# Performance work log

Hardware: AMD Instinct MI355X
Metric: run time of the kernel (lower is better)

## Reference

```python
import jax, jax.numpy as jnp
import numpy as np

EPS = 1e-5

def _layer_norm(x, g, b):
    mu = jnp.mean(x, axis=-1, keepdims=True)
    var = jnp.mean((x - mu) ** 2, axis=-1, keepdims=True)
    return (x - mu) * jax.lax.rsqrt(var + EPS) * g + b


def setup_inputs() -> dict:
    key = jax.random.key(0)
    ks = jax.random.split(key, 16)
    D, F = 768, 3072
    s = 0.02
    def lin(k, din, dout):
        return jax.random.normal(k, (din, dout), jnp.float32) * s
    return {
        "x": jax.random.normal(ks[0], (2, 2048, D), jnp.float32),
        "wq": lin(ks[1], D, D), "bq": jnp.zeros((D,), jnp.float32),
        "wk": lin(ks[2], D, D), "bk": jnp.zeros((D,), jnp.float32),
        "wv": lin(ks[3], D, D), "bv": jnp.zeros((D,), jnp.float32),
        "wo": lin(ks[4], D, D), "bo": jnp.zeros((D,), jnp.float32),
        "w1": lin(ks[5], D, F), "b1": jnp.zeros((F,), jnp.float32),
        "w2": lin(ks[6], F, D), "b2": jnp.zeros((D,), jnp.float32),
        "g1": jnp.ones((D,), jnp.float32), "be1": jnp.zeros((D,), jnp.float32),
        "g2": jnp.ones((D,), jnp.float32), "be2": jnp.zeros((D,), jnp.float32),
    }


def reference(x, wq, bq, wk, bk, wv, bv, wo, bo, w1, b1, w2, b2, g1, be1, g2, be2):
    B, S, D = x.shape
    H = 12
    hd = D // H
    h = _layer_norm(x, g1, be1)
    # project and split heads: [B,S,D] -> [B,H,S,hd]
    def heads(y):
        return y.reshape(B, S, H, hd).transpose(0, 2, 1, 3)
    q = heads(h @ wq + bq)
    k = heads(h @ wk + bk)
    v = heads(h @ wv + bv)
    energy = jnp.einsum("bhqd,bhkd->bhqk", q, k) / np.sqrt(hd).astype(np.float32)
    attention = jax.nn.softmax(energy, axis=-1)
    # NOTE: source bug preserved — uses raw energy (not attention) for AV matmul
    ctx = jnp.einsum("bhqk,bhkd->bhqd", energy, v)
    ctx = ctx.transpose(0, 2, 1, 3).reshape(B, S, D)
    attn_out = ctx @ wo + bo
    x = x + attn_out
    h2 = _layer_norm(x, g2, be2)
    mlp = jax.nn.gelu(h2 @ w1 + b1, approximate=False) @ w2 + b2
    x = x + mlp
    return (x, attention)
```

## Files before the change

### kernel.cpp

```cpp
#include <hip/hip_runtime.h>
#include <cmath>

typedef __bf16 bf16;
typedef __bf16 bf16x8 __attribute__((ext_vector_type(8)));
typedef __bf16 bf16x4v __attribute__((ext_vector_type(4)));
typedef float f32x4 __attribute__((ext_vector_type(4)));

#define DEV __device__ __forceinline__

DEV void gld16(const void* g, void* l) {
  __builtin_amdgcn_global_load_lds((__attribute__((address_space(1))) void*)(g),
                                   (__attribute__((address_space(3))) void*)(l), 16, 0, 0);
}

DEV f32x4 mfma16(bf16x8 a, bf16x8 b, f32x4 c) {
  return __builtin_amdgcn_mfma_f32_16x16x32_bf16(a, b, c, 0, 0, 0);
}

__global__ __launch_bounds__(256) void ln_kernel(const float* __restrict__ x,
    const float* __restrict__ g, const float* __restrict__ be, bf16* __restrict__ h)
{
  const int row = blockIdx.x, t = threadIdx.x;
  const float* xr = x + (size_t)row * 768;
  float v0 = xr[t], v1 = xr[t + 256], v2 = xr[t + 512];
  float s = v0 + v1 + v2;
  float ss = v0 * v0 + v1 * v1 + v2 * v2;
#pragma unroll
  for (int m = 32; m >= 1; m >>= 1) { s += __shfl_xor(s, m); ss += __shfl_xor(ss, m); }
  __shared__ float ps[8];
  const int w = t >> 6;
  if ((t & 63) == 0) { ps[w] = s; ps[4 + w] = ss; }
  __syncthreads();
  s = ps[0] + ps[1] + ps[2] + ps[3];
  ss = ps[4] + ps[5] + ps[6] + ps[7];
  const float mu = s * (1.0f / 768.0f);
  const float var = ss * (1.0f / 768.0f) - mu * mu;
  const float rs = rsqrtf(var + 1e-5f);
  bf16* hr = h + (size_t)row * 768;
  hr[t]       = (bf16)((v0 - mu) * rs * g[t]       + be[t]);
  hr[t + 256] = (bf16)((v1 - mu) * rs * g[t + 256] + be[t + 256]);
  hr[t + 512] = (bf16)((v2 - mu) * rs * g[t + 512] + be[t + 512]);
}

__global__ __launch_bounds__(256) void transpose_w(const float* __restrict__ w,
    bf16* __restrict__ wT, int din, int dout)
{
  __shared__ __align__(16) float tw[64 * 68];
  const int t = threadIdx.x;
  const int n0 = blockIdx.x * 64, k0 = blockIdx.y * 64;
#pragma unroll
  for (int it = 0; it < 4; ++it) {
    const int slot = it * 256 + t;
    const int r = slot >> 4, c = slot & 15;
    *(f32x4*)(tw + r * 68 + c * 4) = *(const f32x4*)(w + (size_t)(k0 + r) * dout + n0 + c * 4);
  }
  __syncthreads();
#pragma unroll
  for (int it = 0; it < 2; ++it) {
    const int slot = it * 256 + t;
    const int n = slot >> 3, c = slot & 7;
    bf16x8 o;
#pragma unroll
    for (int j = 0; j < 8; ++j) o[j] = (bf16)tw[(c * 8 + j) * 68 + n];
    *(bf16x8*)(wT + (size_t)(n0 + n) * din + k0 + c * 8) = o;
  }
}

__global__ __launch_bounds__(256) void transpose_v(const bf16* __restrict__ v, bf16* __restrict__ vT)
{
  __shared__ __align__(16) bf16 tv[64 * 80];
  const int t = threadIdx.x;
  const int s0 = blockIdx.x * 64, bh = blockIdx.y;
  const bf16* vg = v + ((size_t)bh * 2048 + s0) * 64;
#pragma unroll
  for (int it = 0; it < 2; ++it) {
    const int slot = it * 256 + t;
    const int r = slot >> 3, c = slot & 7;
    *(bf16x8*)(tv + r * 80 + c * 8) = *(const bf16x8*)(vg + slot * 8);
  }
  __syncthreads();
  bf16* og = vT + (size_t)bh * 64 * 2048 + s0;
#pragma unroll
  for (int it = 0; it < 2; ++it) {
    const int slot = it * 256 + t;
    const int d = slot >> 3, c = slot & 7;
    bf16x8 o;
#pragma unroll
    for (int j = 0; j < 8; ++j) o[j] = tv[(c * 8 + j) * 80 + d];
    *(bf16x8*)(og + (size_t)d * 2048 + c * 8) = o;
  }
}

template <int MODE>
__global__ __launch_bounds__(256, 2) void gemm_bt(
    const bf16* __restrict__ A, const bf16* __restrict__ B, const int K,
    const float* __restrict__ bias0, const float* __restrict__ bias1,
    const float* __restrict__ bias2, const float* __restrict__ resid,
    float* __restrict__ outf, bf16* __restrict__ outb,
    bf16* __restrict__ kout, bf16* __restrict__ vout)
{
  __shared__ __align__(16) bf16 As[128 * 32];
  __shared__ __align__(16) bf16 Bs[128 * 32];
  const int t = threadIdx.x;
  const int m0 = blockIdx.y * 128, n0 = blockIdx.x * 128;
  const int w = t >> 6, lane = t & 63, l15 = lane & 15, quad = lane >> 4;
  const int wr = (w >> 1) * 64, wc = (w & 1) * 64;

  const f32x4 zero = {0.f, 0.f, 0.f, 0.f};
  f32x4 acc[4][4];
#pragma unroll
  for (int i = 0; i < 4; ++i)
#pragma unroll
    for (int j = 0; j < 4; ++j) acc[i][j] = zero;

  for (int k0 = 0; k0 < K; k0 += 32) {
#pragma unroll
    for (int j = 0; j < 2; ++j) {
      const int slot = j * 256 + t;
      const int row = slot >> 2, kc = slot & 3;
      gld16(A + (size_t)(m0 + row) * K + k0 + kc * 8, As + (size_t)(j * 256 + (t & 192)) * 8);
      gld16(B + (size_t)(n0 + row) * K + k0 + kc * 8, Bs + (size_t)(j * 256 + (t & 192)) * 8);
    }
    __syncthreads();
    bf16x8 af[4], bfr[4];
#pragma unroll
    for (int i = 0; i < 4; ++i) af[i] = *(const bf16x8*)(As + (wr + i * 16 + l15) * 32 + quad * 8);
#pragma unroll
    for (int i = 0; i < 4; ++i) bfr[i] = *(const bf16x8*)(Bs + (wc + i * 16 + l15) * 32 + quad * 8);
#pragma unroll
    for (int mi = 0; mi < 4; ++mi)
#pragma unroll
      for (int ni = 0; ni < 4; ++ni) acc[mi][ni] = mfma16(af[mi], bfr[ni], acc[mi][ni]);
    __syncthreads();
  }

  if constexpr (MODE == 0) {
    const int part = n0 / 768;
    const int cb = n0 - part * 768;
    const float* bp = part == 0 ? bias0 : (part == 1 ? bias1 : bias2);
    bf16* dst = part == 0 ? outb : (part == 1 ? kout : vout);
    float bias[4];
#pragma unroll
    for (int ni = 0; ni < 4; ++ni) bias[ni] = bp[cb + wc + ni * 16 + l15];
#pragma unroll
    for (int mi = 0; mi < 4; ++mi) {
      const int tok = m0 + wr + mi * 16 + quad * 4;
      const int b = tok >> 11, sIdx = tok & 2047;
#pragma unroll
      for (int ni = 0; ni < 4; ++ni) {
        const int c = cb + wc + ni * 16 + l15;
        const int head = c >> 6, d = c & 63;
        bf16* o = dst + (((size_t)b * 12 + head) * 2048 + sIdx) * 64 + d;
#pragma unroll
        for (int r = 0; r < 4; ++r) o[(size_t)r * 64] = (bf16)(acc[mi][ni][r] + bias[ni]);
      }
    }
  } else if constexpr (MODE == 1 || MODE == 3) {
    float bias[4];
#pragma unroll
    for (int ni = 0; ni < 4; ++ni) bias[ni] = bias0[n0 + wc + ni * 16 + l15];
#pragma unroll
    for (int mi = 0; mi < 4; ++mi) {
      const int row = m0 + wr + mi * 16 + quad * 4;
#pragma unroll
      for (int ni = 0; ni < 4; ++ni) {
        const int c = n0 + wc + ni * 16 + l15;
#pragma unroll
        for (int r = 0; r < 4; ++r) {
          const size_t idx = (size_t)(row + r) * 768 + c;
          outf[idx] = resid[idx] + acc[mi][ni][r] + bias[ni];
        }
      }
    }
  } else {
    float bias[4];
#pragma unroll
    for (int ni = 0; ni < 4; ++ni) bias[ni] = bias0[n0 + wc + ni * 16 + l15];
#pragma unroll
    for (int mi = 0; mi < 4; ++mi) {
      const int row = m0 + wr + mi * 16 + quad * 4;
#pragma unroll
      for (int ni = 0; ni < 4; ++ni) {
        const int c = n0 + wc + ni * 16 + l15;
#pragma unroll
        for (int r = 0; r < 4; ++r) {
          const size_t idx = (size_t)(row + r) * 3072 + c;
          const float gv = acc[mi][ni][r] + bias[ni];
          outb[idx] = (bf16)(0.5f * gv * (1.0f + erff(gv * 0.70710678118f)));
        }
      }
    }
  }
}

__global__ __launch_bounds__(256, 2) void attn_kernel(
    const bf16* __restrict__ q, const bf16* __restrict__ k,
    const bf16* __restrict__ vT, bf16* __restrict__ ctx,
    float* __restrict__ energy)
{
  __shared__ __align__(16) bf16 qs[128 * 64];
  __shared__ __align__(16) bf16 ks[64 * 64];
  __shared__ __align__(16) bf16 vs[64 * 64];
  __shared__ __align__(16) bf16 es[128 * 64];
  const int t = threadIdx.x, w = t >> 6, lane = t & 63;
  const int l15 = lane & 15, quad = lane >> 4;
  const int q0 = blockIdx.x * 128, bh = blockIdx.y;
  const int b = bh / 12, head = bh % 12;

  const bf16* qg = q + ((size_t)bh * 2048 + q0) * 64;
#pragma unroll
  for (int j = 0; j < 4; ++j) gld16(qg + (j * 256 + t) * 8, qs + (size_t)(j * 256 + (t & 192)) * 8);

  const f32x4 zero = {0.f, 0.f, 0.f, 0.f};
  f32x4 accc[2][4];
#pragma unroll
  for (int mi = 0; mi < 2; ++mi)
#pragma unroll
    for (int ni = 0; ni < 4; ++ni) accc[mi][ni] = zero;

  for (int kt = 0; kt < 32; ++kt) {
    const bf16* kg = k + ((size_t)bh * 2048 + kt * 64) * 64;
#pragma unroll
    for (int j = 0; j < 2; ++j) gld16(kg + (j * 256 + t) * 8, ks + (size_t)(j * 256 + (t & 192)) * 8);
    const bf16* vg = vT + (size_t)bh * 64 * 2048 + kt * 64;
#pragma unroll
    for (int j = 0; j < 2; ++j) {
      const int slot = j * 256 + t;
      const int d = slot >> 3, c = slot & 7;
      gld16(vg + (size_t)d * 2048 + c * 8, vs + (size_t)(j * 256 + (t & 192)) * 8);
    }
    __syncthreads();

    f32x4 e[2][4];
#pragma unroll
    for (int mi = 0; mi < 2; ++mi)
#pragma unroll
      for (int nj = 0; nj < 4; ++nj) e[mi][nj] = zero;
#pragma unroll
    for (int kk = 0; kk < 2; ++kk) {
      bf16x8 aq[2];
#pragma unroll
      for (int mi = 0; mi < 2; ++mi)
        aq[mi] = *(const bf16x8*)(qs + (w * 32 + mi * 16 + l15) * 64 + kk * 32 + quad * 8);
#pragma unroll
      for (int nj = 0; nj < 4; ++nj) {
        bf16x8 kb8 = *(const bf16x8*)(ks + (nj * 16 + l15) * 64 + kk * 32 + quad * 8);
#pragma unroll
        for (int mi = 0; mi < 2; ++mi) e[mi][nj] = mfma16(aq[mi], kb8, e[mi][nj]);
      }
    }
#pragma unroll
    for (int mi = 0; mi < 2; ++mi)
#pragma unroll
      for (int nj = 0; nj < 4; ++nj)
#pragma unroll
        for (int r = 0; r < 4; ++r)
          es[(w * 32 + mi * 16 + quad * 4 + r) * 64 + nj * 16 + l15] = (bf16)(e[mi][nj][r] * 0.125f);

    float* eg = energy + ((size_t)(bh * 2048 + q0 + w * 32)) * 2048 + kt * 64;
#pragma unroll
    for (int it = 0; it < 8; ++it) {
      const int slot = it * 64 + lane;
      const int r = slot >> 4, c4 = slot & 15;
      bf16x4v ev = *(const bf16x4v*)(es + (w * 32 + r) * 64 + c4 * 4);
      f32x4 o = {(float)ev[0], (float)ev[1], (float)ev[2], (float)ev[3]};
      *(f32x4*)(eg + (size_t)r * 2048 + c4 * 4) = o;
    }

#pragma unroll
    for (int kk = 0; kk < 2; ++kk) {
      bf16x8 ae[2];
#pragma unroll
      for (int mi = 0; mi < 2; ++mi)
        ae[mi] = *(const bf16x8*)(es + (w * 32 + mi * 16 + l15) * 64 + kk * 32 + quad * 8);
#pragma unroll
      for (int ni = 0; ni < 4; ++ni) {
        bf16x8 vb8 = *(const bf16x8*)(vs + (ni * 16 + l15) * 64 + kk * 32 + quad * 8);
#pragma unroll
        for (int mi = 0; mi < 2; ++mi) accc[mi][ni] = mfma16(ae[mi], vb8, accc[mi][ni]);
      }
    }
    __syncthreads();
  }

#pragma unroll
  for (int mi = 0; mi < 2; ++mi) {
    const int srow = q0 + w * 32 + mi * 16 + quad * 4;
#pragma unroll
    for (int ni = 0; ni < 4; ++ni) {
      const int d = ni * 16 + l15;
      bf16* o = ctx + ((size_t)(b * 2048 + srow)) * 768 + head * 64 + d;
#pragma unroll
      for (int r = 0; r < 4; ++r) o[(size_t)r * 768] = (bf16)accc[mi][ni][r];
    }
  }
}

__global__ __launch_bounds__(256) void softmax_kernel(float* __restrict__ att)
{
  const int w = threadIdx.x >> 6, lane = threadIdx.x & 63;
  const size_t row = (size_t)blockIdx.x * 4 + w;
  float* p = att + row * 2048;
  f32x4 v[8];
  float s = 0.f;
#pragma unroll
  for (int c = 0; c < 8; ++c) {
    f32x4 x = *(const f32x4*)(p + c * 256 + lane * 4);
    f32x4 e = {__expf(x[0]), __expf(x[1]), __expf(x[2]), __expf(x[3])};
    v[c] = e;
    s += e[0] + e[1] + e[2] + e[3];
  }
#pragma unroll
  for (int m = 32; m >= 1; m >>= 1) s += __shfl_xor(s, m);
  const float inv = 1.0f / s;
#pragma unroll
  for (int c = 0; c < 8; ++c) {
    f32x4 o = {v[c][0] * inv, v[c][1] * inv, v[c][2] * inv, v[c][3] * inv};
    *(f32x4*)(p + c * 256 + lane * 4) = o;
  }
}

extern "C" void kernel_launch(void* const* d_in, const int* in_sizes, int n_in,
                              void* d_out, int out_size, void* d_ws, size_t ws_size,
                              hipStream_t stream)
{
  const float* x  = (const float*)d_in[0];
  const float* wq = (const float*)d_in[1];
  const float* bq = (const float*)d_in[2];
  const float* wk = (const float*)d_in[3];
  const float* bk = (const float*)d_in[4];
  const float* wv = (const float*)d_in[5];
  const float* bv = (const float*)d_in[6];
  const float* wo = (const float*)d_in[7];
  const float* bo = (const float*)d_in[8];
  const float* w1 = (const float*)d_in[9];
  const float* b1 = (const float*)d_in[10];
  const float* w2 = (const float*)d_in[11];
  const float* b2 = (const float*)d_in[12];
  const float* g1 = (const float*)d_in[13];
  const float* be1 = (const float*)d_in[14];
  const float* g2 = (const float*)d_in[15];
  const float* be2 = (const float*)d_in[16];

  float* out = (float*)d_out;
  float* energy = out + 3145728;

  if (ws_size < (size_t)95944704) return;
  char* ws = (char*)d_ws;
  bf16* wqkvT = (bf16*)(ws + 0);
  bf16* woT   = (bf16*)(ws + 3538944);
  bf16* w1T   = (bf16*)(ws + 4718592);
  bf16* w2T   = (bf16*)(ws + 9437184);
  bf16* h     = (bf16*)(ws + 14155776);
  bf16* qb    = (bf16*)(ws + 20447232);
  bf16* kb    = (bf16*)(ws + 26738688);
  bf16* vb    = (bf16*)(ws + 33030144);
  bf16* vTb   = (bf16*)(ws + 39321600);
  bf16* ctxb  = (bf16*)(ws + 45613056);
  float* x2   = (float*)(ws + 51904512);
  bf16* h2    = (bf16*)(ws + 64487424);
  bf16* a1    = (bf16*)(ws + 70778880);

  transpose_w<<<dim3(12, 12), 256, 0, stream>>>(wq, wqkvT, 768, 768);
  transpose_w<<<dim3(12, 12), 256, 0, stream>>>(wk, wqkvT + 768 * 768, 768, 768);
  transpose_w<<<dim3(12, 12), 256, 0, stream>>>(wv, wqkvT + 2 * 768 * 768, 768, 768);
  transpose_w<<<dim3(12, 12), 256, 0, stream>>>(wo, woT, 768, 768);
  transpose_w<<<dim3(48, 12), 256, 0, stream>>>(w1, w1T, 768, 3072);
  transpose_w<<<dim3(12, 48), 256, 0, stream>>>(w2, w2T, 3072, 768);

  ln_kernel<<<4096, 256, 0, stream>>>(x, g1, be1, h);
  gemm_bt<0><<<dim3(18, 32), 256, 0, stream>>>(h, wqkvT, 768, bq, bk, bv,
                                               nullptr, nullptr, qb, kb, vb);
  transpose_v<<<dim3(32, 24), 256, 0, stream>>>(vb, vTb);
  attn_kernel<<<dim3(16, 24), 256, 0, stream>>>(qb, kb, vTb, ctxb, energy);
  softmax_kernel<<<12288, 256, 0, stream>>>(energy);
  gemm_bt<1><<<dim3(6, 32), 256, 0, stream>>>(ctxb, woT, 768, bo, nullptr, nullptr,
                                              x, x2, nullptr, nullptr, nullptr);
  ln_kernel<<<4096, 256, 0, stream>>>(x2, g2, be2, h2);
  gemm_bt<2><<<dim3(24, 32), 256, 0, stream>>>(h2, w1T, 768, b1, nullptr, nullptr,
                                               nullptr, nullptr, a1, nullptr, nullptr);
  gemm_bt<3><<<dim3(6, 32), 256, 0, stream>>>(a1, w2T, 3072, b2, nullptr, nullptr,
                                              x2, out, nullptr, nullptr, nullptr);
}
```

Baseline: 842.0 us.

## Fuse softmax into two-pass attention, split-K the W2 GEMM, batch weight transposes

Removes the separate softmax kernel. The attention kernel now accumulates row exp-sums in a first pass over K/V, then recomputes QK^T in a second pass and writes normalized probabilities directly. This saves a full fp32 read-modify-write of the 2048x2048 attention matrix, at the cost of running the QK^T MFMAs twice. The W2 GEMM is split along K into two halves to double the grid size, and a reduce kernel adds the partials, bias and residual. The four 768x768 weight transposes are merged into one launch.

```diff
diff --git a/kernel.cpp b/kernel.cpp
--- a/kernel.cpp
+++ b/kernel.cpp
@@ -42,17 +42,16 @@
   hr[t + 512] = (bf16)((v2 - mu) * rs * g[t + 512] + be[t + 512]);
 }
 
-__global__ __launch_bounds__(256) void transpose_w(const float* __restrict__ w,
-    bf16* __restrict__ wT, int din, int dout)
+template <int DIN, int DOUT>
+DEV void transpose_body(const float* __restrict__ w, bf16* __restrict__ wT,
+                        int n0, int k0, int t)
 {
   __shared__ __align__(16) float tw[64 * 68];
-  const int t = threadIdx.x;
-  const int n0 = blockIdx.x * 64, k0 = blockIdx.y * 64;
 #pragma unroll
   for (int it = 0; it < 4; ++it) {
     const int slot = it * 256 + t;
     const int r = slot >> 4, c = slot & 15;
-    *(f32x4*)(tw + r * 68 + c * 4) = *(const f32x4*)(w + (size_t)(k0 + r) * dout + n0 + c * 4);
+    *(f32x4*)(tw + r * 68 + c * 4) = *(const f32x4*)(w + (size_t)(k0 + r) * DOUT + n0 + c * 4);
   }
   __syncthreads();
 #pragma unroll
@@ -62,8 +61,26 @@
     bf16x8 o;
 #pragma unroll
     for (int j = 0; j < 8; ++j) o[j] = (bf16)tw[(c * 8 + j) * 68 + n];
-    *(bf16x8*)(wT + (size_t)(n0 + n) * din + k0 + c * 8) = o;
-  }
+    *(bf16x8*)(wT + (size_t)(n0 + n) * DIN + k0 + c * 8) = o;
+  }
+}
+
+__global__ __launch_bounds__(256) void transpose_w4(
+    const float* __restrict__ a, const float* __restrict__ b,
+    const float* __restrict__ c, const float* __restrict__ d,
+    bf16* __restrict__ qkvT, bf16* __restrict__ oT)
+{
+  const int z = blockIdx.z;
+  const float* w = z == 0 ? a : (z == 1 ? b : (z == 2 ? c : d));
+  bf16* dst = z < 3 ? qkvT + (size_t)z * 768 * 768 : oT;
+  transpose_body<768, 768>(w, dst, blockIdx.x * 64, blockIdx.y * 64, threadIdx.x);
+}
+
+template <int DIN, int DOUT>
+__global__ __launch_bounds__(256) void transpose_w(const float* __restrict__ w,
+    bf16* __restrict__ wT)
+{
+  transpose_body<DIN, DOUT>(w, wT, blockIdx.x * 64, blockIdx.y * 64, threadIdx.x);
 }
 
 __global__ __launch_bounds__(256) void transpose_v(const bf16* __restrict__ v, bf16* __restrict__ vT)
@@ -75,8 +92,7 @@
 #pragma unroll
   for (int it = 0; it < 2; ++it) {
     const int slot = it * 256 + t;
-    const int r = slot >> 3, c = slot & 7;
-    *(bf16x8*)(tv + r * 80 + c * 8) = *(const bf16x8*)(vg + slot * 8);
+    *(bf16x8*)(tv + (slot >> 3) * 80 + (slot & 7) * 8) = *(const bf16x8*)(vg + slot * 8);
   }
   __syncthreads();
   bf16* og = vT + (size_t)bh * 64 * 2048 + s0;
@@ -93,7 +109,8 @@
 
 template <int MODE>
 __global__ __launch_bounds__(256, 2) void gemm_bt(
-    const bf16* __restrict__ A, const bf16* __restrict__ B, const int K,
+    const bf16* __restrict__ A, const bf16* __restrict__ B,
+    const int K, const int Kstride,
     const float* __restrict__ bias0, const float* __restrict__ bias1,
     const float* __restrict__ bias2, const float* __restrict__ resid,
     float* __restrict__ outf, bf16* __restrict__ outb,
@@ -103,6 +120,7 @@
   __shared__ __align__(16) bf16 Bs[128 * 32];
   const int t = threadIdx.x;
   const int m0 = blockIdx.y * 128, n0 = blockIdx.x * 128;
+  const int kOff = (MODE == 4) ? blockIdx.z * K : 0;
   const int w = t >> 6, lane = t & 63, l15 = lane & 15, quad = lane >> 4;
   const int wr = (w >> 1) * 64, wc = (w & 1) * 64;
 
@@ -118,8 +136,10 @@
     for (int j = 0; j < 2; ++j) {
       const int slot = j * 256 + t;
       const int row = slot >> 2, kc = slot & 3;
-      gld16(A + (size_t)(m0 + row) * K + k0 + kc * 8, As + (size_t)(j * 256 + (t & 192)) * 8);
-      gld16(B + (size_t)(n0 + row) * K + k0 + kc * 8, Bs + (size_t)(j * 256 + (t & 192)) * 8);
+      gld16(A + (size_t)(m0 + row) * Kstride + kOff + k0 + kc * 8,
+            As + (size_t)(j * 256 + (t & 192)) * 8);
+      gld16(B + (size_t)(n0 + row) * Kstride + kOff + k0 + kc * 8,
+            Bs + (size_t)(j * 256 + (t & 192)) * 8);
     }
     __syncthreads();
     bf16x8 af[4], bfr[4];
@@ -172,7 +192,7 @@
         }
       }
     }
-  } else {
+  } else if constexpr (MODE == 2) {
     float bias[4];
 #pragma unroll
     for (int ni = 0; ni < 4; ++ni) bias[ni] = bias0[n0 + wc + ni * 16 + l15];
@@ -190,18 +210,45 @@
         }
       }
     }
-  }
+  } else {
+    float* op = outf + (size_t)blockIdx.z * 3145728;
+#pragma unroll
+    for (int mi = 0; mi < 4; ++mi) {
+      const int row = m0 + wr + mi * 16 + quad * 4;
+#pragma unroll
+      for (int ni = 0; ni < 4; ++ni) {
+        const int c = n0 + wc + ni * 16 + l15;
+#pragma unroll
+        for (int r = 0; r < 4; ++r) op[(size_t)(row + r) * 768 + c] = acc[mi][ni][r];
+      }
+    }
+  }
+}
+
+__global__ __launch_bounds__(256) void reduce_w2(const float* __restrict__ p0,
+    const float* __restrict__ p1, const float* __restrict__ resid,
+    const float* __restrict__ bias, float* __restrict__ out)
+{
+  const size_t i = ((size_t)blockIdx.x * 256 + threadIdx.x) * 4;
+  f32x4 a = *(const f32x4*)(p0 + i);
+  f32x4 b = *(const f32x4*)(p1 + i);
+  f32x4 r = *(const f32x4*)(resid + i);
+  f32x4 bb = *(const f32x4*)(bias + (i & 767));
+  f32x4 o = {r[0] + a[0] + b[0] + bb[0], r[1] + a[1] + b[1] + bb[1],
+             r[2] + a[2] + b[2] + bb[2], r[3] + a[3] + b[3] + bb[3]};
+  *(f32x4*)(out + i) = o;
 }
 
 __global__ __launch_bounds__(256, 2) void attn_kernel(
     const bf16* __restrict__ q, const bf16* __restrict__ k,
     const bf16* __restrict__ vT, bf16* __restrict__ ctx,
-    float* __restrict__ energy)
+    float* __restrict__ att)
 {
   __shared__ __align__(16) bf16 qs[128 * 64];
   __shared__ __align__(16) bf16 ks[64 * 64];
   __shared__ __align__(16) bf16 vs[64 * 64];
   __shared__ __align__(16) bf16 es[128 * 64];
+  __shared__ float rsum[128];
   const int t = threadIdx.x, w = t >> 6, lane = t & 63;
   const int l15 = lane & 15, quad = lane >> 4;
   const int q0 = blockIdx.x * 128, bh = blockIdx.y;
@@ -213,10 +260,11 @@
 
   const f32x4 zero = {0.f, 0.f, 0.f, 0.f};
   f32x4 accc[2][4];
+  float psum[2][4];
 #pragma unroll
   for (int mi = 0; mi < 2; ++mi)
 #pragma unroll
-    for (int ni = 0; ni < 4; ++ni) accc[mi][ni] = zero;
+    for (int ni = 0; ni < 4; ++ni) { accc[mi][ni] = zero; psum[mi][ni] = 0.f; }
 
   for (int kt = 0; kt < 32; ++kt) {
     const bf16* kg = k + ((size_t)bh * 2048 + kt * 64) * 64;
@@ -226,8 +274,7 @@
 #pragma unroll
     for (int j = 0; j < 2; ++j) {
       const int slot = j * 256 + t;
-      const int d = slot >> 3, c = slot & 7;
-      gld16(vg + (size_t)d * 2048 + c * 8, vs + (size_t)(j * 256 + (t & 192)) * 8);
+      gld16(vg + (size_t)(slot >> 3) * 2048 + (slot & 7) * 8, vs + (size_t)(j * 256 + (t & 192)) * 8);
     }
     __syncthreads();
 
@@ -254,69 +301,98 @@
 #pragma unroll
       for (int nj = 0; nj < 4; ++nj)
 #pragma unroll
+        for (int r = 0; r < 4; ++r) {
+          const bf16 eb = (bf16)(e[mi][nj][r] * 0.125f);
+          es[(w * 32 + mi * 16 + quad * 4 + r) * 64 + nj * 16 + l15] = eb;
+          psum[mi][r] += __expf((float)eb);
+        }
+
+#pragma unroll
+    for (int kk = 0; kk < 2; ++kk) {
+      bf16x8 ae[2];
+#pragma unroll
+      for (int mi = 0; mi < 2; ++mi)
+        ae[mi] = *(const bf16x8*)(es + (w * 32 + mi * 16 + l15) * 64 + kk * 32 + quad * 8);
+#pragma unroll
+      for (int ni = 0; ni < 4; ++ni) {
+        bf16x8 vb8 = *(const bf16x8*)(vs + (ni * 16 + l15) * 64 + kk * 32 + quad * 8);
+#pragma unroll
+        for (int mi = 0; mi < 2; ++mi) accc[mi][ni] = mfma16(ae[mi], vb8, accc[mi][ni]);
+      }
+    }
+    __syncthreads();
+  }
+
+#pragma unroll
+  for (int mi = 0; mi < 2; ++mi)
+#pragma unroll
+    for (int r = 0; r < 4; ++r) {
+      float s = psum[mi][r];
+#pragma unroll
+      for (int m = 8; m >= 1; m >>= 1) s += __shfl_xor(s, m);
+      if (l15 == 0) rsum[w * 32 + mi * 16 + quad * 4 + r] = s;
+    }
+  __syncthreads();
+
+#pragma unroll
+  for (int mi = 0; mi < 2; ++mi) {
+    const int srow = q0 + w * 32 + mi * 16 + quad * 4;
+#pragma unroll
+    for (int ni = 0; ni < 4; ++ni) {
+      const int d = ni * 16 + l15;
+      bf16* o = ctx + ((size_t)(b * 2048 + srow)) * 768 + head * 64 + d;
+#pragma unroll
+      for (int r = 0; r < 4; ++r) o[(size_t)r * 768] = (bf16)accc[mi][ni][r];
+    }
+  }
+
+  float inv[8];
+#pragma unroll
+  for (int it = 0; it < 8; ++it) inv[it] = 1.0f / rsum[w * 32 + it * 4 + quad];
+
+  for (int kt = 0; kt < 32; ++kt) {
+    const bf16* kg = k + ((size_t)bh * 2048 + kt * 64) * 64;
+#pragma unroll
+    for (int j = 0; j < 2; ++j) gld16(kg + (j * 256 + t) * 8, ks + (size_t)(j * 256 + (t & 192)) * 8);
+    __syncthreads();
+
+    f32x4 e[2][4];
+#pragma unroll
+    for (int mi = 0; mi < 2; ++mi)
+#pragma unroll
+      for (int nj = 0; nj < 4; ++nj) e[mi][nj] = zero;
+#pragma unroll
+    for (int kk = 0; kk < 2; ++kk) {
+      bf16x8 aq[2];
+#pragma unroll
+      for (int mi = 0; mi < 2; ++mi)
+        aq[mi] = *(const bf16x8*)(qs + (w * 32 + mi * 16 + l15) * 64 + kk * 32 + quad * 8);
+#pragma unroll
+      for (int nj = 0; nj < 4; ++nj) {
+        bf16x8 kb8 = *(const bf16x8*)(ks + (nj * 16 + l15) * 64 + kk * 32 + quad * 8);
+#pragma unroll
+        for (int mi = 0; mi < 2; ++mi) e[mi][nj] = mfma16(aq[mi], kb8, e[mi][nj]);
+      }
+    }
+#pragma unroll
+    for (int mi = 0; mi < 2; ++mi)
+#pragma unroll
+      for (int nj = 0; nj < 4; ++nj)
+#pragma unroll
         for (int r = 0; r < 4; ++r)
           es[(w * 32 + mi * 16 + quad * 4 + r) * 64 + nj * 16 + l15] = (bf16)(e[mi][nj][r] * 0.125f);
 
-    float* eg = energy + ((size_t)(bh * 2048 + q0 + w * 32)) * 2048 + kt * 64;
+    float* eg = att + ((size_t)(bh * 2048 + q0 + w * 32)) * 2048 + kt * 64;
 #pragma unroll
     for (int it = 0; it < 8; ++it) {
       const int slot = it * 64 + lane;
       const int r = slot >> 4, c4 = slot & 15;
       bf16x4v ev = *(const bf16x4v*)(es + (w * 32 + r) * 64 + c4 * 4);
-      f32x4 o = {(float)ev[0], (float)ev[1], (float)ev[2], (float)ev[3]};
+      f32x4 o = {__expf((float)ev[0]) * inv[it], __expf((float)ev[1]) * inv[it],
+                 __expf((float)ev[2]) * inv[it], __expf((float)ev[3]) * inv[it]};
       *(f32x4*)(eg + (size_t)r * 2048 + c4 * 4) = o;
     }
-
-#pragma unroll
-    for (int kk = 0; kk < 2; ++kk) {
-      bf16x8 ae[2];
-#pragma unroll
-      for (int mi = 0; mi < 2; ++mi)
-        ae[mi] = *(const bf16x8*)(es + (w * 32 + mi * 16 + l15) * 64 + kk * 32 + quad * 8);
-#pragma unroll
-      for (int ni = 0; ni < 4; ++ni) {
-        bf16x8 vb8 = *(const bf16x8*)(vs + (ni * 16 + l15) * 64 + kk * 32 + quad * 8);
-#pragma unroll
-        for (int mi = 0; mi < 2; ++mi) accc[mi][ni] = mfma16(ae[mi], vb8, accc[mi][ni]);
-      }
-    }
-    __syncthreads();
-  }
-
-#pragma unroll
-  for (int mi = 0; mi < 2; ++mi) {
-    const int srow = q0 + w * 32 + mi * 16 + quad * 4;
-#pragma unroll
-    for (int ni = 0; ni < 4; ++ni) {
-      const int d = ni * 16 + l15;
-      bf16* o = ctx + ((size_t)(b * 2048 + srow)) * 768 + head * 64 + d;
-#pragma unroll
-      for (int r = 0; r < 4; ++r) o[(size_t)r * 768] = (bf16)accc[mi][ni][r];
-    }
-  }
-}
-
-__global__ __launch_bounds__(256) void softmax_kernel(float* __restrict__ att)
-{
-  const int w = threadIdx.x >> 6, lane = threadIdx.x & 63;
-  const size_t row = (size_t)blockIdx.x * 4 + w;
-  float* p = att + row * 2048;
-  f32x4 v[8];
-  float s = 0.f;
-#pragma unroll
-  for (int c = 0; c < 8; ++c) {
-    f32x4 x = *(const f32x4*)(p + c * 256 + lane * 4);
-    f32x4 e = {__expf(x[0]), __expf(x[1]), __expf(x[2]), __expf(x[3])};
-    v[c] = e;
-    s += e[0] + e[1] + e[2] + e[3];
-  }
-#pragma unroll
-  for (int m = 32; m >= 1; m >>= 1) s += __shfl_xor(s, m);
-  const float inv = 1.0f / s;
-#pragma unroll
-  for (int c = 0; c < 8; ++c) {
-    f32x4 o = {v[c][0] * inv, v[c][1] * inv, v[c][2] * inv, v[c][3] * inv};
-    *(f32x4*)(p + c * 256 + lane * 4) = o;
+    __syncthreads();
   }
 }
 
@@ -343,7 +419,7 @@
   const float* be2 = (const float*)d_in[16];
 
   float* out = (float*)d_out;
-  float* energy = out + 3145728;
+  float* att = out + 3145728;
 
   if (ws_size < (size_t)95944704) return;
   char* ws = (char*)d_ws;
@@ -360,25 +436,23 @@
   float* x2   = (float*)(ws + 51904512);
   bf16* h2    = (bf16*)(ws + 64487424);
   bf16* a1    = (bf16*)(ws + 70778880);
-
-  transpose_w<<<dim3(12, 12), 256, 0, stream>>>(wq, wqkvT, 768, 768);
-  transpose_w<<<dim3(12, 12), 256, 0, stream>>>(wk, wqkvT + 768 * 768, 768, 768);
-  transpose_w<<<dim3(12, 12), 256, 0, stream>>>(wv, wqkvT + 2 * 768 * 768, 768, 768);
-  transpose_w<<<dim3(12, 12), 256, 0, stream>>>(wo, woT, 768, 768);
-  transpose_w<<<dim3(48, 12), 256, 0, stream>>>(w1, w1T, 768, 3072);
-  transpose_w<<<dim3(12, 48), 256, 0, stream>>>(w2, w2T, 3072, 768);
+  float* w2p  = (float*)(ws + 20447232);
+
+  transpose_w4<<<dim3(12, 12, 4), 256, 0, stream>>>(wq, wk, wv, wo, wqkvT, woT);
+  transpose_w<768, 3072><<<dim3(48, 12), 256, 0, stream>>>(w1, w1T);
+  transpose_w<3072, 768><<<dim3(12, 48), 256, 0, stream>>>(w2, w2T);
 
   ln_kernel<<<4096, 256, 0, stream>>>(x, g1, be1, h);
-  gemm_bt<0><<<dim3(18, 32), 256, 0, stream>>>(h, wqkvT, 768, bq, bk, bv,
+  gemm_bt<0><<<dim3(18, 32), 256, 0, stream>>>(h, wqkvT, 768, 768, bq, bk, bv,
                                                nullptr, nullptr, qb, kb, vb);
   transpose_v<<<dim3(32, 24), 256, 0, stream>>>(vb, vTb);
-  attn_kernel<<<dim3(16, 24), 256, 0, stream>>>(qb, kb, vTb, ctxb, energy);
-  softmax_kernel<<<12288, 256, 0, stream>>>(energy);
-  gemm_bt<1><<<dim3(6, 32), 256, 0, stream>>>(ctxb, woT, 768, bo, nullptr, nullptr,
+  attn_kernel<<<dim3(16, 24), 256, 0, stream>>>(qb, kb, vTb, ctxb, att);
+  gemm_bt<1><<<dim3(6, 32), 256, 0, stream>>>(ctxb, woT, 768, 768, bo, nullptr, nullptr,
                                               x, x2, nullptr, nullptr, nullptr);
   ln_kernel<<<4096, 256, 0, stream>>>(x2, g2, be2, h2);
-  gemm_bt<2><<<dim3(24, 32), 256, 0, stream>>>(h2, w1T, 768, b1, nullptr, nullptr,
+  gemm_bt<2><<<dim3(24, 32), 256, 0, stream>>>(h2, w1T, 768, 768, b1, nullptr, nullptr,
                                                nullptr, nullptr, a1, nullptr, nullptr);
-  gemm_bt<3><<<dim3(6, 32), 256, 0, stream>>>(a1, w2T, 3072, b2, nullptr, nullptr,
-                                              x2, out, nullptr, nullptr, nullptr);
-}
+  gemm_bt<4><<<dim3(6, 32, 2), 256, 0, stream>>>(a1, w2T, 1536, 3072, nullptr, nullptr,
+                                                 nullptr, nullptr, w2p, nullptr, nullptr, nullptr);
+  reduce_w2<<<3072, 256, 0, stream>>>(w2p, w2p + 3145728, x2, b2, out);
+}
```

Measured after the change: 732.4 us. 1.15x faster.
